# Kernel optimization log

Measured on AMD Instinct MI355X. Metric: run time of the kernel, lower is better.

The kernel has to match this reference:

```python
import jax, jax.numpy as jnp
import numpy as np

T = 2048          # tokens (single causal prefill sequence)
H = 4096          # hidden_size
NH = 32           # num query heads
NKV = 8           # num kv heads (GQA)
HD = H // NH      # head_dim = 128
ROPE_THETA = 500000.0
Q_SIZE = NH * HD
KV_SIZE = NKV * HD


def setup_inputs() -> dict:
    key = jax.random.key(0)
    k1, k2, k3 = jax.random.split(key, 3)
    return {
        "positions": jnp.arange(T, dtype=jnp.int32),
        "hidden_states": jax.random.normal(k1, (T, H), dtype=jnp.float32) * 0.02,
        "w_qkv": jax.random.normal(k2, (H, Q_SIZE + 2 * KV_SIZE), dtype=jnp.float32) * (1.0 / np.sqrt(H)),
        "w_o": jax.random.normal(k3, (Q_SIZE, H), dtype=jnp.float32) * (1.0 / np.sqrt(Q_SIZE)),
    }


def _apply_rope(x, positions):
    # x: [T, heads, HD]; neox-style (non-interleaved) RoPE as in get_rope
    half = HD // 2
    inv_freq = 1.0 / (ROPE_THETA ** (jnp.arange(0, half, dtype=jnp.float32) / half * 1.0))
    # note: standard llama uses arange(0, HD, 2)/HD == arange(half)/half
    freqs = positions.astype(jnp.float32)[:, None] * inv_freq[None, :]   # [T, half]
    cos = jnp.cos(freqs)[:, None, :]  # [T, 1, half]
    sin = jnp.sin(freqs)[:, None, :]
    x1, x2 = x[..., :half], x[..., half:]
    return jnp.concatenate([x1 * cos - x2 * sin, x2 * cos + x1 * sin], axis=-1).astype(x.dtype)


def reference(positions, hidden_states, w_qkv, w_o):
    # qkv_proj (no bias)
    qkv = hidden_states @ w_qkv                               # [T, 6144]
    q, k, v = jnp.split(qkv, [Q_SIZE, Q_SIZE + KV_SIZE], axis=-1)
    q = q.reshape(T, NH, HD)
    k = k.reshape(T, NKV, HD)
    v = v.reshape(T, NKV, HD)

    # fused RoPE on q and k (k would be written rotated into the KV cache)
    q = _apply_rope(q, positions)
    k = _apply_rope(k, positions)

    # GQA: expand kv heads to query heads
    group = NH // NKV
    k_rep = jnp.repeat(k, group, axis=1)                      # [T, NH, HD]
    v_rep = jnp.repeat(v, group, axis=1)

    scale = HD ** -0.5
    scores = jnp.einsum('qhd,shd->hqs', q, k_rep) * scale     # [NH, T, T]
    causal = jnp.tril(jnp.ones((T, T), dtype=bool))
    scores = jnp.where(causal[None], scores, jnp.finfo(scores.dtype).min)
    probs = jax.nn.softmax(scores, axis=-1)
    attn = jnp.einsum('hqs,shd->qhd', probs, v_rep)           # [T, NH, HD]

    out = attn.reshape(T, Q_SIZE) @ w_o                       # o_proj
    return out
```

## Files before the change

kernel.cpp:

```cpp
#include <hip/hip_runtime.h>
#include <cstdint>
#include <cstddef>

#define T_SEQ 2048
#define H_DIM 4096
#define NH 32
#define NKV 8
#define HD 128
#define QKV_N 6144
#define Q_SIZE 4096
#define KV_SIZE 1024

typedef __attribute__((ext_vector_type(8))) short bf16x8;
typedef __attribute__((ext_vector_type(4))) short short4v;
typedef __attribute__((ext_vector_type(4))) float f32x4;

__device__ __forceinline__ short f2bf(float f) {
  union { float f; uint32_t u; } v; v.f = f;
  uint32_t r = v.u + 0x7fffu + ((v.u >> 16) & 1u);
  return (short)(r >> 16);
}

__device__ __forceinline__ void gload_lds16(const void* g, void* l) {
  __builtin_amdgcn_global_load_lds((const __attribute__((address_space(1))) void*)g,
                                   (__attribute__((address_space(3))) void*)l,
                                   16, 0, 0);
}

__global__ __launch_bounds__(256) void cvt_bf16_kernel(const float* __restrict__ in,
                                                       short* __restrict__ out, int n4) {
  int i = blockIdx.x * 256 + threadIdx.x;
  if (i < n4) {
    float4 v = ((const float4*)in)[i];
    short4v s;
    s.x = f2bf(v.x); s.y = f2bf(v.y); s.z = f2bf(v.z); s.w = f2bf(v.w);
    ((short4v*)out)[i] = s;
  }
}

__global__ __launch_bounds__(256) void zero_f4_kernel(float* __restrict__ p, int n4) {
  int i = blockIdx.x * 256 + threadIdx.x;
  int stride = gridDim.x * 256;
  float4 z = {0.f, 0.f, 0.f, 0.f};
  for (; i < n4; i += stride) ((float4*)p)[i] = z;
}

__global__ __launch_bounds__(256) void transpose_cvt64_kernel(const float* __restrict__ in,
                                                              short* __restrict__ out,
                                                              int rows, int cols) {
  __shared__ float tile[64][65];
  int bx = blockIdx.x * 64;
  int by = blockIdx.y * 64;
  int t = threadIdx.x;
  int lr = t >> 4;
  int lc4 = t & 15;
#pragma unroll
  for (int p = 0; p < 4; ++p) {
    int r = p * 16 + lr;
    float4 v = *(const float4*)(in + (size_t)(by + r) * cols + bx + lc4 * 4);
    tile[r][lc4 * 4 + 0] = v.x; tile[r][lc4 * 4 + 1] = v.y;
    tile[r][lc4 * 4 + 2] = v.z; tile[r][lc4 * 4 + 3] = v.w;
  }
  __syncthreads();
  int w = t >> 6, l = t & 63;
  int colg = l >> 3;
  int rseg = (l & 7) * 8;
#pragma unroll
  for (int p = 0; p < 2; ++p) {
    int col = (p * 4 + w) * 8 + colg;
    bf16x8 r8;
#pragma unroll
    for (int i = 0; i < 8; ++i) r8[i] = f2bf(tile[rseg + i][col]);
    *(bf16x8*)(out + (size_t)(bx + col) * rows + by + rseg) = r8;
  }
}

#define BARRIER() do { __builtin_amdgcn_s_barrier(); \
                       __builtin_amdgcn_sched_barrier(0); \
                       asm volatile("" ::: "memory"); } while (0)
#define VMCNT4() asm volatile("s_waitcnt vmcnt(4)" ::: "memory")
#define PRIO1 __builtin_amdgcn_s_setprio(1)
#define PRIO0 __builtin_amdgcn_s_setprio(0)

#define LDA_HALF(BASE, MH) do { \
  _Pragma("unroll") \
  for (int m_ = 0; m_ < 4; ++m_) { \
    _Pragma("unroll") \
    for (int ks_ = 0; ks_ < 2; ++ks_) { \
      int row_ = arow + (MH) * 64 + m_ * 16 + l16; \
      aF[m_][ks_] = *(const bf16x8*)((BASE) + row_ * 64 + (((ks_ * 4 + quad) ^ (row_ & 7)) << 3)); \
    } } } while (0)

#define LDB_HALF(BASE, NH, DST) do { \
  _Pragma("unroll") \
  for (int n_ = 0; n_ < 2; ++n_) { \
    _Pragma("unroll") \
    for (int ks_ = 0; ks_ < 2; ++ks_) { \
      int row_ = brow + (NH) * 32 + n_ * 16 + l16; \
      (DST)[n_][ks_] = *(const bf16x8*)((BASE) + row_ * 64 + (((ks_ * 4 + quad) ^ (row_ & 7)) << 3)); \
    } } } while (0)

#define MMQ(MH, NH, BF) do { \
  _Pragma("unroll") \
  for (int m_ = 0; m_ < 4; ++m_) { \
    _Pragma("unroll") \
    for (int n_ = 0; n_ < 2; ++n_) { \
      _Pragma("unroll") \
      for (int ks_ = 0; ks_ < 2; ++ks_) \
        acc[(MH) * 4 + m_][(NH) * 2 + n_] = __builtin_amdgcn_mfma_f32_16x16x32_bf16( \
            aF[m_][ks_], (BF)[n_][ks_], acc[(MH) * 4 + m_][(NH) * 2 + n_], 0, 0, 0); \
    } } } while (0)

__device__ __forceinline__ void stage_half(const short* __restrict__ src, int ldk,
                                           short* dst, int half, int tid) {
#pragma unroll
  for (int q = 0; q < 2; ++q) {
    int cc = half * 1024 + q * 512 + tid;
    int row = cc >> 3, cq = cc & 7;
    gload_lds16(src + (size_t)row * ldk + ((cq ^ (row & 7)) << 3), dst + cc * 8);
  }
}

__global__ __launch_bounds__(512, 1) void gemm_bt256_kernel(const short* __restrict__ A,
                                                            const short* __restrict__ Bt,
                                                            float* __restrict__ C,
                                                            int M, int N, int K,
                                                            int klen) {
  __shared__ short lds[65536];
  short* As0 = lds;
  short* Bs0 = lds + 16384;
  short* As1 = lds + 32768;
  short* Bs1 = lds + 49152;
  int tid = threadIdx.x;
  int w = tid >> 6, lane = tid & 63;
  int quad = lane >> 4, l16 = lane & 15;
  int wr = w >> 2, wc = w & 3;
  int arow = wr * 128, brow = wc * 64;
  int bm = blockIdx.y * 256, bn = blockIdx.x * 256;
  int k0 = blockIdx.z * klen;
  const short* Asrc = A + (size_t)bm * K + k0;
  const short* Bsrc = Bt + (size_t)bn * K + k0;
  int NT = klen >> 6, NI = NT >> 1;

  f32x4 acc[8][4] = {};
  bf16x8 aF[4][2], b0F[2][2], b1F[2][2];

  stage_half(Asrc, K, As0, 0, tid);
  stage_half(Asrc, K, As0, 1, tid);
  stage_half(Bsrc, K, Bs0, 0, tid);
  stage_half(Bsrc, K, Bs0, 1, tid);
  stage_half(Bsrc + 64, K, Bs1, 0, tid);
  stage_half(Bsrc + 64, K, Bs1, 1, tid);
  VMCNT4();
  BARRIER();

#pragma unroll 1
  for (int i = 0; i < NI; ++i) {
    const short* a1 = Asrc + (size_t)(2 * i + 1) * 64;
    int kt2 = 2 * i + 2; if (kt2 > NT - 1) kt2 = NT - 1;
    int kt3 = 2 * i + 3; if (kt3 > NT - 1) kt3 = NT - 1;
    const short* a2 = Asrc + (size_t)kt2 * 64;
    const short* b2 = Bsrc + (size_t)kt2 * 64;
    const short* b3 = Bsrc + (size_t)kt3 * 64;

    LDA_HALF(As0, 0);
    LDB_HALF(Bs0, 0, b0F);
    stage_half(a1, K, As1, 0, tid);
    BARRIER();
    PRIO1; MMQ(0, 0, b0F); PRIO0;
    BARRIER();
    LDB_HALF(Bs0, 1, b1F);
    stage_half(a1, K, As1, 1, tid);
    BARRIER();
    PRIO1; MMQ(0, 1, b1F); PRIO0;
    BARRIER();
    LDA_HALF(As0, 1);
    stage_half(b2, K, Bs0, 0, tid);
    BARRIER();
    PRIO1; MMQ(1, 1, b1F); PRIO0;
    BARRIER();
    stage_half(b2, K, Bs0, 1, tid);
    BARRIER();
    PRIO1; MMQ(1, 0, b0F); PRIO0;
    VMCNT4();
    BARRIER();
    LDA_HALF(As1, 0);
    LDB_HALF(Bs1, 0, b0F);
    stage_half(a2, K, As0, 0, tid);
    BARRIER();
    PRIO1; MMQ(0, 0, b0F); PRIO0;
    BARRIER();
    LDB_HALF(Bs1, 1, b1F);
    stage_half(a2, K, As0, 1, tid);
    BARRIER();
    PRIO1; MMQ(0, 1, b1F); PRIO0;
    BARRIER();
    LDA_HALF(As1, 1);
    stage_half(b3, K, Bs1, 0, tid);
    BARRIER();
    PRIO1; MMQ(1, 1, b1F); PRIO0;
    BARRIER();
    stage_half(b3, K, Bs1, 1, tid);
    BARRIER();
    PRIO1; MMQ(1, 0, b0F); PRIO0;
    VMCNT4();
    BARRIER();
  }
  asm volatile("s_waitcnt vmcnt(0)" ::: "memory");

  if (gridDim.z > 1) {
#pragma unroll
    for (int mi = 0; mi < 8; ++mi)
#pragma unroll
      for (int ni = 0; ni < 4; ++ni) {
        int r0 = bm + arow + mi * 16 + quad * 4;
        int c0 = bn + brow + ni * 16 + l16;
#pragma unroll
        for (int r = 0; r < 4; ++r)
          atomicAdd(&C[(size_t)(r0 + r) * N + c0], acc[mi][ni][r]);
      }
  } else {
#pragma unroll
    for (int mi = 0; mi < 8; ++mi)
#pragma unroll
      for (int ni = 0; ni < 4; ++ni) {
        int r0 = bm + arow + mi * 16 + quad * 4;
        int c0 = bn + brow + ni * 16 + l16;
#pragma unroll
        for (int r = 0; r < 4; ++r)
          C[(size_t)(r0 + r) * N + c0] = acc[mi][ni][r];
      }
  }
}

__global__ __launch_bounds__(256) void rope_kernel(const float* __restrict__ qkv,
                                                   const int* __restrict__ positions,
                                                   short* __restrict__ qb,
                                                   short* __restrict__ kb) {
  int t = blockIdx.x;
  int hh = blockIdx.y * 4 + (threadIdx.x >> 6);
  int j = threadIdx.x & 63;
  float pos = (float)positions[t];
  float f = pos * exp2f(-(float)j * 0.29580575889569017f);
  float c = cosf(f), sn = sinf(f);
  size_t rowbase = (size_t)t * QKV_N;
  int coloff = (hh < NH) ? hh * HD : Q_SIZE + (hh - NH) * HD;
  float x1 = qkv[rowbase + coloff + j];
  float x2 = qkv[rowbase + coloff + j + 64];
  float o1 = x1 * c - x2 * sn;
  float o2 = x2 * c + x1 * sn;
  const float scale2 = 0.08838834764831845f * 1.4426950408889634f;
  short* dst;
  if (hh < NH) {
    o1 *= scale2; o2 *= scale2;
    dst = qb + ((size_t)hh * T_SEQ + t) * HD;
  } else {
    dst = kb + ((size_t)(hh - NH) * T_SEQ + t) * HD;
  }
  dst[j] = f2bf(o1);
  dst[j + 64] = f2bf(o2);
}

__global__ __launch_bounds__(256) void transpose_v_kernel(const float* __restrict__ qkv,
                                                          short* __restrict__ vt) {
  __shared__ float tile[32][33];
  int bx = blockIdx.x * 32;
  int by = blockIdx.y * 32;
  int x = threadIdx.x, y = threadIdx.y;
#pragma unroll
  for (int i = 0; i < 32; i += 8)
    tile[y + i][x] = qkv[(size_t)(by + y + i) * QKV_N + (Q_SIZE + KV_SIZE) + bx + x];
  __syncthreads();
#pragma unroll
  for (int i = 0; i < 32; i += 8)
    vt[(size_t)(bx + y + i) * T_SEQ + by + x] = f2bf(tile[x][y + i]);
}

#define PS_STR 72
__global__ __launch_bounds__(256, 2) void flash_kernel(const short* __restrict__ qb,
                                                       const short* __restrict__ kb,
                                                       const short* __restrict__ vt,
                                                       short* __restrict__ attn) {
  __shared__ short Ks[64 * 128];
  __shared__ short Vs[128 * 64];
  __shared__ short Ps[8][16 * PS_STR];
  int c = (int)gridDim.x - 1 - (int)blockIdx.x;
  int h = blockIdx.y;
  int kvh = h >> 2;
  int tid = threadIdx.x;
  int w = tid >> 6, lane = tid & 63;
  int quad = lane >> 4, l16 = lane & 15;
  int qrow0w = c * 128 + w * 32;

  const short* kbh = kb + (size_t)kvh * T_SEQ * HD;
  const short* vth = vt + (size_t)kvh * HD * T_SEQ;

  bf16x8 qf[2][4];
#pragma unroll
  for (int g = 0; g < 2; ++g) {
    const short* qbase = qb + ((size_t)h * T_SEQ + qrow0w + g * 16 + l16) * HD + quad * 8;
#pragma unroll
    for (int dk = 0; dk < 4; ++dk) qf[g][dk] = *(const bf16x8*)(qbase + dk * 32);
  }
  f32x4 o[2][8] = {};
  float lp[2] = {0.0f, 0.0f};

  int ktmax_blk = 2 * c + 2;
  int ktmax_w = 2 * c + 1 + (w >> 1);

  for (int kt = 0; kt < ktmax_blk; ++kt) {
    int kpos0 = kt * 64;
    __syncthreads();
#pragma unroll
    for (int p4 = 0; p4 < 4; ++p4) {
      int e = p4 * 256 + tid;
      int kr = e >> 4, kp = e & 15;
      gload_lds16(kbh + (size_t)(kpos0 + kr) * HD + ((kp ^ (kr & 7)) * 8), Ks + e * 8);
      int vd = e >> 3, vp = e & 7;
      gload_lds16(vth + (size_t)vd * T_SEQ + kpos0 + ((vp ^ (vd & 7)) * 8), Vs + e * 8);
    }
    __syncthreads();
    if (kt >= ktmax_w) continue;

    f32x4 s[2][4] = {};
#pragma unroll
    for (int mi = 0; mi < 4; ++mi) {
      int kr = mi * 16 + l16;
      const short* kfb = Ks + kr * 128;
      int sw = kr & 7;
#pragma unroll
      for (int dk = 0; dk < 4; ++dk) {
        bf16x8 kf = *(const bf16x8*)(kfb + (((dk * 4 + quad) ^ sw) * 8));
        s[0][mi] = __builtin_amdgcn_mfma_f32_16x16x32_bf16(kf, qf[0][dk], s[0][mi], 0, 0, 0);
        s[1][mi] = __builtin_amdgcn_mfma_f32_16x16x32_bf16(kf, qf[1][dk], s[1][mi], 0, 0, 0);
      }
    }
#pragma unroll
    for (int g = 0; g < 2; ++g) {
      int qr = qrow0w + g * 16 + l16;
      bool need_mask = (kpos0 + 63 > qrow0w + g * 16);
#pragma unroll
      for (int mi = 0; mi < 4; ++mi) {
        float p0, p1, p2, p3;
        if (need_mask) {
          int kp = kpos0 + mi * 16 + quad * 4;
          p0 = exp2f((kp + 0 > qr) ? -1e30f : s[g][mi][0]);
          p1 = exp2f((kp + 1 > qr) ? -1e30f : s[g][mi][1]);
          p2 = exp2f((kp + 2 > qr) ? -1e30f : s[g][mi][2]);
          p3 = exp2f((kp + 3 > qr) ? -1e30f : s[g][mi][3]);
        } else {
          p0 = exp2f(s[g][mi][0]); p1 = exp2f(s[g][mi][1]);
          p2 = exp2f(s[g][mi][2]); p3 = exp2f(s[g][mi][3]);
        }
        lp[g] += p0 + p1 + p2 + p3;
        short4v pk;
        pk.x = f2bf(p0); pk.y = f2bf(p1); pk.z = f2bf(p2); pk.w = f2bf(p3);
        *(short4v*)(&Ps[w * 2 + g][l16 * PS_STR + mi * 16 + quad * 4]) = pk;
      }
    }
#pragma unroll
    for (int kf2 = 0; kf2 < 2; ++kf2) {
      bf16x8 pf0 = *(const bf16x8*)(&Ps[w * 2 + 0][l16 * PS_STR + kf2 * 32 + quad * 8]);
      bf16x8 pf1 = *(const bf16x8*)(&Ps[w * 2 + 1][l16 * PS_STR + kf2 * 32 + quad * 8]);
#pragma unroll
      for (int ni = 0; ni < 8; ++ni) {
        int vd = ni * 16 + l16;
        bf16x8 vf = *(const bf16x8*)(Vs + vd * 64 + (((kf2 * 4 + quad) ^ (vd & 7)) * 8));
        o[0][ni] = __builtin_amdgcn_mfma_f32_16x16x32_bf16(vf, pf0, o[0][ni], 0, 0, 0);
        o[1][ni] = __builtin_amdgcn_mfma_f32_16x16x32_bf16(vf, pf1, o[1][ni], 0, 0, 0);
      }
    }
  }
#pragma unroll
  for (int g = 0; g < 2; ++g) {
    float lt = lp[g];
    lt += __shfl_xor(lt, 16, 64);
    lt += __shfl_xor(lt, 32, 64);
    float rl = 1.0f / lt;
    short* dst = attn + (size_t)(qrow0w + g * 16 + l16) * Q_SIZE + h * HD + quad * 4;
#pragma unroll
    for (int ni = 0; ni < 8; ++ni) {
      short4v ov;
      ov.x = f2bf(o[g][ni][0] * rl); ov.y = f2bf(o[g][ni][1] * rl);
      ov.z = f2bf(o[g][ni][2] * rl); ov.w = f2bf(o[g][ni][3] * rl);
      *(short4v*)(dst + ni * 16) = ov;
    }
  }
}

extern "C" void kernel_launch(void* const* d_in, const int* in_sizes, int n_in,
                              void* d_out, int out_size, void* d_ws, size_t ws_size,
                              hipStream_t stream) {
  const int* positions = (const int*)d_in[0];
  const float* hidden  = (const float*)d_in[1];
  const float* w_qkv   = (const float*)d_in[2];
  const float* w_o     = (const float*)d_in[3];
  float* out = (float*)d_out;

  char* p = (char*)d_ws;
  short* hA    = (short*)p;               short* attn = hA;
  p += (size_t)T_SEQ * H_DIM * 2;
  short* wqkvT = (short*)p;
  p += (size_t)QKV_N * H_DIM * 2;
  float* qkv   = (float*)p;               short* woT = (short*)p;
  short* qb = wqkvT;
  short* kb = qb + (size_t)NH * T_SEQ * HD;
  short* vt = kb + (size_t)NKV * T_SEQ * HD;

  cvt_bf16_kernel<<<dim3(T_SEQ * H_DIM / 4 / 256), 256, 0, stream>>>(hidden, hA, T_SEQ * H_DIM / 4);
  transpose_cvt64_kernel<<<dim3(QKV_N / 64, H_DIM / 64), 256, 0, stream>>>(w_qkv, wqkvT, H_DIM, QKV_N);
  gemm_bt256_kernel<<<dim3(QKV_N / 256, T_SEQ / 256, 1), 512, 0, stream>>>(hA, wqkvT, qkv, T_SEQ, QKV_N, H_DIM, H_DIM);
  rope_kernel<<<dim3(T_SEQ, (NH + NKV) / 4), 256, 0, stream>>>(qkv, positions, qb, kb);
  transpose_v_kernel<<<dim3(KV_SIZE / 32, T_SEQ / 32), dim3(32, 8), 0, stream>>>(qkv, vt);
  transpose_cvt64_kernel<<<dim3(H_DIM / 64, H_DIM / 64), 256, 0, stream>>>(w_o, woT, H_DIM, H_DIM);
  flash_kernel<<<dim3(T_SEQ / 128, NH), 256, 0, stream>>>(qb, kb, vt, attn);
  zero_f4_kernel<<<dim3(2048), 256, 0, stream>>>(out, T_SEQ * H_DIM / 4);
  gemm_bt256_kernel<<<dim3(H_DIM / 256, T_SEQ / 256, 2), 512, 0, stream>>>(attn, woT, out, T_SEQ, H_DIM, H_DIM, H_DIM / 2);
}
```

Before: 545.0 us.

## Replace split-K atomic o_proj GEMM with 128x256 tiles and direct stores

Templates the GEMM on the per-warp M extent so the o_proj GEMM can use 128x256 output tiles instead of 256x256 tiles with split-K. This keeps the block count at 256 while dropping the zero-fill kernel and the atomicAdd epilogue in favour of plain stores. Each block now runs the full K loop, which means twice as many K iterations per block with smaller A tiles and less reuse per loaded B tile. The QKV GEMM keeps its previous configuration.

```diff
diff --git a/kernel.cpp b/kernel.cpp
--- a/kernel.cpp
+++ b/kernel.cpp
@@ -36,13 +36,6 @@
     s.x = f2bf(v.x); s.y = f2bf(v.y); s.z = f2bf(v.z); s.w = f2bf(v.w);
     ((short4v*)out)[i] = s;
   }
-}
-
-__global__ __launch_bounds__(256) void zero_f4_kernel(float* __restrict__ p, int n4) {
-  int i = blockIdx.x * 256 + threadIdx.x;
-  int stride = gridDim.x * 256;
-  float4 z = {0.f, 0.f, 0.f, 0.f};
-  for (; i < n4; i += stride) ((float4*)p)[i] = z;
 }
 
 __global__ __launch_bounds__(256) void transpose_cvt64_kernel(const float* __restrict__ in,
@@ -84,73 +77,76 @@
 
 #define LDA_HALF(BASE, MH) do { \
   _Pragma("unroll") \
-  for (int m_ = 0; m_ < 4; ++m_) { \
+  for (int m_ = 0; m_ < MF; ++m_) { \
     _Pragma("unroll") \
     for (int ks_ = 0; ks_ < 2; ++ks_) { \
-      int row_ = arow + (MH) * 64 + m_ * 16 + l16; \
+      int row_ = arow + (MH) * (WM / 2) + m_ * 16 + l16; \
       aF[m_][ks_] = *(const bf16x8*)((BASE) + row_ * 64 + (((ks_ * 4 + quad) ^ (row_ & 7)) << 3)); \
     } } } while (0)
 
-#define LDB_HALF(BASE, NH, DST) do { \
+#define LDB_HALF(BASE, NHH, DST) do { \
   _Pragma("unroll") \
   for (int n_ = 0; n_ < 2; ++n_) { \
     _Pragma("unroll") \
     for (int ks_ = 0; ks_ < 2; ++ks_) { \
-      int row_ = brow + (NH) * 32 + n_ * 16 + l16; \
+      int row_ = brow + (NHH) * 32 + n_ * 16 + l16; \
       (DST)[n_][ks_] = *(const bf16x8*)((BASE) + row_ * 64 + (((ks_ * 4 + quad) ^ (row_ & 7)) << 3)); \
     } } } while (0)
 
-#define MMQ(MH, NH, BF) do { \
+#define MMQ(MH, NHH, BF) do { \
   _Pragma("unroll") \
-  for (int m_ = 0; m_ < 4; ++m_) { \
+  for (int m_ = 0; m_ < MF; ++m_) { \
     _Pragma("unroll") \
     for (int n_ = 0; n_ < 2; ++n_) { \
       _Pragma("unroll") \
       for (int ks_ = 0; ks_ < 2; ++ks_) \
-        acc[(MH) * 4 + m_][(NH) * 2 + n_] = __builtin_amdgcn_mfma_f32_16x16x32_bf16( \
-            aF[m_][ks_], (BF)[n_][ks_], acc[(MH) * 4 + m_][(NH) * 2 + n_], 0, 0, 0); \
+        acc[(MH) * MF + m_][(NHH) * 2 + n_] = __builtin_amdgcn_mfma_f32_16x16x32_bf16( \
+            aF[m_][ks_], (BF)[n_][ks_], acc[(MH) * MF + m_][(NHH) * 2 + n_], 0, 0, 0); \
     } } } while (0)
 
+template<int L>
 __device__ __forceinline__ void stage_half(const short* __restrict__ src, int ldk,
                                            short* dst, int half, int tid) {
 #pragma unroll
-  for (int q = 0; q < 2; ++q) {
-    int cc = half * 1024 + q * 512 + tid;
+  for (int q = 0; q < L; ++q) {
+    int cc = half * (512 * L) + q * 512 + tid;
     int row = cc >> 3, cq = cc & 7;
     gload_lds16(src + (size_t)row * ldk + ((cq ^ (row & 7)) << 3), dst + cc * 8);
   }
 }
 
+template<int WM>
 __global__ __launch_bounds__(512, 1) void gemm_bt256_kernel(const short* __restrict__ A,
                                                             const short* __restrict__ Bt,
                                                             float* __restrict__ C,
-                                                            int M, int N, int K,
-                                                            int klen) {
-  __shared__ short lds[65536];
+                                                            int M, int N, int K) {
+  constexpr int MF = WM / 32;
+  constexpr int AL = WM / 64;
+  constexpr int ASH = WM * 128;
+  __shared__ short lds[2 * (ASH + 16384)];
   short* As0 = lds;
-  short* Bs0 = lds + 16384;
-  short* As1 = lds + 32768;
-  short* Bs1 = lds + 49152;
+  short* Bs0 = lds + ASH;
+  short* As1 = Bs0 + 16384;
+  short* Bs1 = As1 + ASH;
   int tid = threadIdx.x;
   int w = tid >> 6, lane = tid & 63;
   int quad = lane >> 4, l16 = lane & 15;
   int wr = w >> 2, wc = w & 3;
-  int arow = wr * 128, brow = wc * 64;
-  int bm = blockIdx.y * 256, bn = blockIdx.x * 256;
-  int k0 = blockIdx.z * klen;
-  const short* Asrc = A + (size_t)bm * K + k0;
-  const short* Bsrc = Bt + (size_t)bn * K + k0;
-  int NT = klen >> 6, NI = NT >> 1;
-
-  f32x4 acc[8][4] = {};
-  bf16x8 aF[4][2], b0F[2][2], b1F[2][2];
-
-  stage_half(Asrc, K, As0, 0, tid);
-  stage_half(Asrc, K, As0, 1, tid);
-  stage_half(Bsrc, K, Bs0, 0, tid);
-  stage_half(Bsrc, K, Bs0, 1, tid);
-  stage_half(Bsrc + 64, K, Bs1, 0, tid);
-  stage_half(Bsrc + 64, K, Bs1, 1, tid);
+  int arow = wr * WM, brow = wc * 64;
+  int bm = blockIdx.y * (2 * WM), bn = blockIdx.x * 256;
+  const short* Asrc = A + (size_t)bm * K;
+  const short* Bsrc = Bt + (size_t)bn * K;
+  int NT = K >> 6, NI = NT >> 1;
+
+  f32x4 acc[2 * MF][4] = {};
+  bf16x8 aF[MF][2], b0F[2][2], b1F[2][2];
+
+  stage_half<AL>(Asrc, K, As0, 0, tid);
+  stage_half<AL>(Asrc, K, As0, 1, tid);
+  stage_half<2>(Bsrc, K, Bs0, 0, tid);
+  stage_half<2>(Bsrc, K, Bs0, 1, tid);
+  stage_half<2>(Bsrc + 64, K, Bs1, 0, tid);
+  stage_half<2>(Bsrc + 64, K, Bs1, 1, tid);
   VMCNT4();
   BARRIER();
 
@@ -165,42 +161,42 @@
 
     LDA_HALF(As0, 0);
     LDB_HALF(Bs0, 0, b0F);
-    stage_half(a1, K, As1, 0, tid);
+    stage_half<AL>(a1, K, As1, 0, tid);
     BARRIER();
     PRIO1; MMQ(0, 0, b0F); PRIO0;
     BARRIER();
     LDB_HALF(Bs0, 1, b1F);
-    stage_half(a1, K, As1, 1, tid);
+    stage_half<AL>(a1, K, As1, 1, tid);
     BARRIER();
     PRIO1; MMQ(0, 1, b1F); PRIO0;
     BARRIER();
     LDA_HALF(As0, 1);
-    stage_half(b2, K, Bs0, 0, tid);
+    stage_half<2>(b2, K, Bs0, 0, tid);
     BARRIER();
     PRIO1; MMQ(1, 1, b1F); PRIO0;
     BARRIER();
-    stage_half(b2, K, Bs0, 1, tid);
+    stage_half<2>(b2, K, Bs0, 1, tid);
     BARRIER();
     PRIO1; MMQ(1, 0, b0F); PRIO0;
     VMCNT4();
     BARRIER();
     LDA_HALF(As1, 0);
     LDB_HALF(Bs1, 0, b0F);
-    stage_half(a2, K, As0, 0, tid);
+    stage_half<AL>(a2, K, As0, 0, tid);
     BARRIER();
     PRIO1; MMQ(0, 0, b0F); PRIO0;
     BARRIER();
     LDB_HALF(Bs1, 1, b1F);
-    stage_half(a2, K, As0, 1, tid);
+    stage_half<AL>(a2, K, As0, 1, tid);
     BARRIER();
     PRIO1; MMQ(0, 1, b1F); PRIO0;
     BARRIER();
     LDA_HALF(As1, 1);
-    stage_half(b3, K, Bs1, 0, tid);
+    stage_half<2>(b3, K, Bs1, 0, tid);
     BARRIER();
     PRIO1; MMQ(1, 1, b1F); PRIO0;
     BARRIER();
-    stage_half(b3, K, Bs1, 1, tid);
+    stage_half<2>(b3, K, Bs1, 1, tid);
     BARRIER();
     PRIO1; MMQ(1, 0, b0F); PRIO0;
     VMCNT4();
@@ -208,29 +204,16 @@
   }
   asm volatile("s_waitcnt vmcnt(0)" ::: "memory");
 
-  if (gridDim.z > 1) {
-#pragma unroll
-    for (int mi = 0; mi < 8; ++mi)
-#pragma unroll
-      for (int ni = 0; ni < 4; ++ni) {
-        int r0 = bm + arow + mi * 16 + quad * 4;
-        int c0 = bn + brow + ni * 16 + l16;
-#pragma unroll
-        for (int r = 0; r < 4; ++r)
-          atomicAdd(&C[(size_t)(r0 + r) * N + c0], acc[mi][ni][r]);
-      }
-  } else {
-#pragma unroll
-    for (int mi = 0; mi < 8; ++mi)
-#pragma unroll
-      for (int ni = 0; ni < 4; ++ni) {
-        int r0 = bm + arow + mi * 16 + quad * 4;
-        int c0 = bn + brow + ni * 16 + l16;
-#pragma unroll
-        for (int r = 0; r < 4; ++r)
-          C[(size_t)(r0 + r) * N + c0] = acc[mi][ni][r];
-      }
-  }
+#pragma unroll
+  for (int mi = 0; mi < 2 * MF; ++mi)
+#pragma unroll
+    for (int ni = 0; ni < 4; ++ni) {
+      int r0 = bm + arow + mi * 16 + quad * 4;
+      int c0 = bn + brow + ni * 16 + l16;
+#pragma unroll
+      for (int r = 0; r < 4; ++r)
+        C[(size_t)(r0 + r) * N + c0] = acc[mi][ni][r];
+    }
 }
 
 __global__ __launch_bounds__(256) void rope_kernel(const float* __restrict__ qkv,
@@ -409,11 +392,10 @@
 
   cvt_bf16_kernel<<<dim3(T_SEQ * H_DIM / 4 / 256), 256, 0, stream>>>(hidden, hA, T_SEQ * H_DIM / 4);
   transpose_cvt64_kernel<<<dim3(QKV_N / 64, H_DIM / 64), 256, 0, stream>>>(w_qkv, wqkvT, H_DIM, QKV_N);
-  gemm_bt256_kernel<<<dim3(QKV_N / 256, T_SEQ / 256, 1), 512, 0, stream>>>(hA, wqkvT, qkv, T_SEQ, QKV_N, H_DIM, H_DIM);
+  gemm_bt256_kernel<128><<<dim3(QKV_N / 256, T_SEQ / 256), 512, 0, stream>>>(hA, wqkvT, qkv, T_SEQ, QKV_N, H_DIM);
   rope_kernel<<<dim3(T_SEQ, (NH + NKV) / 4), 256, 0, stream>>>(qkv, positions, qb, kb);
   transpose_v_kernel<<<dim3(KV_SIZE / 32, T_SEQ / 32), dim3(32, 8), 0, stream>>>(qkv, vt);
   transpose_cvt64_kernel<<<dim3(H_DIM / 64, H_DIM / 64), 256, 0, stream>>>(w_o, woT, H_DIM, H_DIM);
   flash_kernel<<<dim3(T_SEQ / 128, NH), 256, 0, stream>>>(qb, kb, vt, attn);
-  zero_f4_kernel<<<dim3(2048), 256, 0, stream>>>(out, T_SEQ * H_DIM / 4);
-  gemm_bt256_kernel<<<dim3(H_DIM / 256, T_SEQ / 256, 2), 512, 0, stream>>>(attn, woT, out, T_SEQ, H_DIM, H_DIM, H_DIM / 2);
-}
+  gemm_bt256_kernel<64><<<dim3(H_DIM / 256, T_SEQ / 128), 512, 0, stream>>>(attn, woT, out, T_SEQ, H_DIM, H_DIM);
+}
```

Measured after the change: 500.3 us. 8.2% less time.
